# Kernel tuning notes

Measured on AMD Instinct MI355X. Metric: run time of the kernel, lower is better.

The kernel has to match this reference:

```python
import jax, jax.numpy as jnp
import numpy as np

N_NODES = 100000
N_EDGES = 1600000
INPUT_DIM = 128
HIDDEN = 128
OUTPUT_DIM = 2
NUM_LAYERS = 2
MAX_RECURSION = 10
TAU_THRESHOLD = 0.005


def setup_inputs() -> dict:
    key = jax.random.key(0)
    ks = jax.random.split(key, 16)
    s = 0.05
    x = jax.random.normal(ks[0], (N_NODES, INPUT_DIM), dtype=jnp.float32)
    edge_index = jax.random.randint(ks[1], (2, N_EDGES), 0, N_NODES, dtype=jnp.int64)
    W_in = jax.random.normal(ks[2], (HIDDEN, INPUT_DIM), dtype=jnp.float32) * s
    b_in = jax.random.normal(ks[3], (HIDDEN,), dtype=jnp.float32) * s
    Wd = jax.random.normal(ks[4], (NUM_LAYERS, HIDDEN, 2 * HIDDEN), dtype=jnp.float32) * s
    bd = jax.random.normal(ks[5], (NUM_LAYERS, HIDDEN), dtype=jnp.float32) * s
    Wt = jax.random.normal(ks[6], (1, HIDDEN), dtype=jnp.float32) * s
    bt = jax.random.normal(ks[7], (1,), dtype=jnp.float32) * s
    W_ih = jax.random.normal(ks[8], (3 * HIDDEN, HIDDEN), dtype=jnp.float32) * s
    W_hh = jax.random.normal(ks[9], (3 * HIDDEN, HIDDEN), dtype=jnp.float32) * s
    b_ih = jax.random.normal(ks[10], (3 * HIDDEN,), dtype=jnp.float32) * s
    b_hh = jax.random.normal(ks[11], (3 * HIDDEN,), dtype=jnp.float32) * s
    Wo = jax.random.normal(ks[12], (OUTPUT_DIM, HIDDEN), dtype=jnp.float32) * s
    bo = jax.random.normal(ks[13], (OUTPUT_DIM,), dtype=jnp.float32) * s
    return dict(x=x, edge_index=edge_index, W_in=W_in, b_in=b_in, Wd=Wd, bd=bd,
                Wt=Wt, bt=bt, W_ih=W_ih, W_hh=W_hh, b_ih=b_ih, b_hh=b_hh, Wo=Wo, bo=bo)


def _gru_cell(x, h, W_ih, W_hh, b_ih, b_hh):
    # torch.nn.GRUCell math
    gi = x @ W_ih.T + b_ih  # [N, 3H]
    gh = h @ W_hh.T + b_hh
    i_r, i_z, i_n = jnp.split(gi, 3, axis=-1)
    h_r, h_z, h_n = jnp.split(gh, 3, axis=-1)
    r = jax.nn.sigmoid(i_r + h_r)
    z = jax.nn.sigmoid(i_z + h_z)
    n = jnp.tanh(i_n + r * h_n)
    return (1.0 - z) * n + z * h


def reference(x, edge_index, W_in, b_in, Wd, bd, Wt, bt, W_ih, W_hh, b_ih, b_hh, Wo, bo):
    N = x.shape[0]
    row, col = edge_index[0], edge_index[1]
    h = jax.nn.relu(x @ W_in.T + b_in)  # [N, H]
    tau = None
    for l in range(NUM_LAYERS):
        diff = jnp.abs(h[row] - h[col])  # [E, H]
        diff_agg = jax.ops.segment_sum(diff, row, num_segments=N)  # [N, H]
        h = jax.nn.relu(jnp.concatenate([h, diff_agg], axis=-1) @ Wd[l].T + bd[l])
        tau = jax.nn.softplus(h @ Wt.T + bt).squeeze(-1)  # [N]
        # n_updates = clamp(floor(1/tau), max=MAX_RECURSION); node updated iff
        # n_updates > 0 and tau < TAU_THRESHOLD. The original inner loop applies
        # gru(diff_agg[i], h[i]) with the ORIGINAL h[i] each iteration, so repeated
        # application is idempotent -> single masked GRU step is exact same math.
        n_updates = jnp.minimum(jnp.floor(1.0 / tau).astype(jnp.int32), MAX_RECURSION)
        mask = (n_updates > 0) & (tau < TAU_THRESHOLD)
        h_gru = _gru_cell(diff_agg, h, W_ih, W_hh, b_ih, b_hh)
        h = jnp.where(mask[:, None], h_gru, h)
    out = h @ Wo.T + bo  # [N, OUTPUT_DIM]
    return out, tau
```

## Files before the change

kernel.cpp:

```cpp
#include <hip/hip_runtime.h>
#include <cstdint>
#include <cstddef>

#define HID 128
#define BSHIFT 7
#define NSB 256
#define MAXB 4096


__global__ __launch_bounds__(256)
void ecount_kernel(const int* __restrict__ row, int* __restrict__ countsT,
                   int E, int nbuck,
                   const float* __restrict__ W_in, const float* __restrict__ Wd,
                   const float* __restrict__ W_ih, const float* __restrict__ W_hh,
                   float* __restrict__ WinT, float* __restrict__ WdT0,
                   float* __restrict__ WdT1, float* __restrict__ WihT,
                   float* __restrict__ WhhT) {
  for (int i = blockIdx.x * 256 + threadIdx.x; i < 180224; i += NSB * 256) {
    int j = i;
    if (j < 16384) { int r = j >> 7, c = j & 127; WinT[c * 128 + r] = W_in[j]; continue; }
    j -= 16384;
    if (j < 32768) { int r = j >> 8, c = j & 255; WdT0[c * 128 + r] = Wd[j]; continue; }
    j -= 32768;
    if (j < 32768) { int r = j >> 8, c = j & 255; WdT1[c * 128 + r] = Wd[32768 + j]; continue; }
    j -= 32768;
    if (j < 49152) { int r = j >> 7, c = j & 127; WihT[c * 384 + r] = W_ih[j]; continue; }
    j -= 49152;
    { int r = j >> 7, c = j & 127; WhhT[c * 384 + r] = W_hh[j]; }
  }
  __shared__ int lh[1024];
  int b = blockIdx.x;
  for (int i = threadIdx.x; i < nbuck; i += 256) lh[i] = 0;
  __syncthreads();
  int per = (E + NSB - 1) / NSB;
  int s = b * per, e = min(s + per, E);
  for (int i = s + (int)threadIdx.x; i < e; i += 256)
    atomicAdd(&lh[row[i] >> BSHIFT], 1);
  __syncthreads();
  for (int i = threadIdx.x; i < nbuck; i += 256) countsT[i * NSB + b] = lh[i];
}

__global__ __launch_bounds__(NSB)
void bprefix_kernel(int* __restrict__ countsT, int* __restrict__ btotal, int nbuck) {
  __shared__ int sd[NSB];
  int bk = blockIdx.x;
  int t = threadIdx.x;
  int v = countsT[bk * NSB + t];
  sd[t] = v;
  __syncthreads();
  for (int off = 1; off < NSB; off <<= 1) {
    int u = (t >= off) ? sd[t - off] : 0;
    __syncthreads();
    sd[t] += u;
    __syncthreads();
  }
  countsT[bk * NSB + t] = sd[t] - v;
  if (t == NSB - 1) btotal[bk] = sd[t];
}

__global__ __launch_bounds__(1024)
void bstart_kernel(const int* __restrict__ btotal, int* __restrict__ bstart,
                   int* __restrict__ offsets, int N, int nbuck) {
  __shared__ int sd[1024];
  int t = threadIdx.x;
  int v = (t < nbuck) ? btotal[t] : 0;
  sd[t] = v;
  __syncthreads();
  for (int off = 1; off < 1024; off <<= 1) {
    int u = (t >= off) ? sd[t - off] : 0;
    __syncthreads();
    sd[t] += u;
    __syncthreads();
  }
  if (t < nbuck) bstart[t] = sd[t] - v;
  if (t == nbuck - 1) { bstart[nbuck] = sd[t]; offsets[N] = sd[t]; }
}

__global__ __launch_bounds__(256)
void escatter_kernel(const int* __restrict__ row, const int* __restrict__ col,
                     const int* __restrict__ countsT, const int* __restrict__ bstart,
                     int2* __restrict__ ebuf, int E, int nbuck) {
  __shared__ int lcur[1024];
  int b = blockIdx.x;
  for (int i = threadIdx.x; i < nbuck; i += 256)
    lcur[i] = bstart[i] + countsT[i * NSB + b];
  __syncthreads();
  int per = (E + NSB - 1) / NSB;
  int s = b * per, e = min(s + per, E);
  for (int i = s + (int)threadIdx.x; i < e; i += 256) {
    int r = row[i], c = col[i];
    int pos = atomicAdd(&lcur[r >> BSHIFT], 1);
    ebuf[pos] = make_int2(r, c);
  }
}

__global__ __launch_bounds__(256)
void bsort_gin_kernel(const int2* __restrict__ ebuf, const int* __restrict__ bstart,
                      int* __restrict__ offsets, int* __restrict__ csr_col,
                      int N, int nbuck,
                      const float* __restrict__ A, const float* __restrict__ BT,
                      const float* __restrict__ bias, float* __restrict__ C, int G) {
  __shared__ union {
    struct { int cnt[128]; int off[128]; int cur[128]; int lcol[MAXB]; } s;
    struct { float As[32][68]; float Bs[32][128]; } g;
  } sm;
  int bid = blockIdx.x;
  int tid = threadIdx.x;
  if (bid < nbuck) {
    int bk = bid;
    int s = bstart[bk], e = bstart[bk + 1];
    int m = e - s;
    if (tid < 128) sm.s.cnt[tid] = 0;
    __syncthreads();
    for (int i = s + tid; i < e; i += 256)
      atomicAdd(&sm.s.cnt[ebuf[i].x & 127], 1);
    __syncthreads();
    if (tid < 128) sm.s.off[tid] = sm.s.cnt[tid];
    __syncthreads();
    for (int d = 1; d < 128; d <<= 1) {
      int v = 0;
      if (tid < 128 && tid >= d) v = sm.s.off[tid - d];
      __syncthreads();
      if (tid < 128) sm.s.off[tid] += v;
      __syncthreads();
    }
    if (tid < 128) {
      sm.s.cur[tid] = sm.s.off[tid] - sm.s.cnt[tid];
      int node = (bk << BSHIFT) + tid;
      if (node < N) offsets[node] = s + sm.s.off[tid] - sm.s.cnt[tid];
    }
    __syncthreads();
    if (m <= MAXB) {
      for (int i = s + tid; i < e; i += 256) {
        int2 rc = ebuf[i];
        int pos = atomicAdd(&sm.s.cur[rc.x & 127], 1);
        sm.s.lcol[pos] = rc.y;
      }
      __syncthreads();
      if (tid < 128) {
        int b0 = sm.s.off[tid] - sm.s.cnt[tid], b1 = sm.s.off[tid];
        for (int i = b0 + 1; i < b1; ++i) {
          int key = sm.s.lcol[i];
          int j = i - 1;
          while (j >= b0 && sm.s.lcol[j] > key) { sm.s.lcol[j + 1] = sm.s.lcol[j]; --j; }
          sm.s.lcol[j + 1] = key;
        }
      }
      __syncthreads();
      for (int i = tid; i < m; i += 256) csr_col[s + i] = sm.s.lcol[i];
    } else {
      for (int i = s + tid; i < e; i += 256) {
        int2 rc = ebuf[i];
        int pos = atomicAdd(&sm.s.cur[rc.x & 127], 1);
        csr_col[s + pos] = rc.y;
      }
    }
    return;
  }
  int tile = bid - nbuck;
  if (tile >= G) return;
  int tx = tid & 31;
  int ty = tid >> 5;
  int i0 = tile * 64;
  int M = N;
  float acc[8][4] = {};
  for (int kc = 0; kc < 4; ++kc) {
    int ksrc = kc * 32;
    #pragma unroll
    for (int q = 0; q < 2; ++q) {
      int f = q * 256 + tid;
      int i = f >> 3;
      int kq = (f & 7) << 2;
      int ig = i0 + i; if (ig >= M) ig = M - 1;
      float4 v = *(const float4*)(A + (size_t)ig * HID + ksrc + kq);
      sm.g.As[kq + 0][i] = v.x; sm.g.As[kq + 1][i] = v.y;
      sm.g.As[kq + 2][i] = v.z; sm.g.As[kq + 3][i] = v.w;
    }
    #pragma unroll
    for (int q = 0; q < 4; ++q) {
      int f = q * 256 + tid;
      int k = f >> 5; int c4 = (f & 31) << 2;
      *(float4*)&sm.g.Bs[k][c4] = *(const float4*)(BT + (size_t)(ksrc + k) * HID + c4);
    }
    __syncthreads();
    #pragma unroll
    for (int k = 0; k < 32; ++k) {
      float a[8];
      const float4* ap = (const float4*)&sm.g.As[k][ty * 8];
      float4 a0 = ap[0], a1 = ap[1];
      a[0]=a0.x; a[1]=a0.y; a[2]=a0.z; a[3]=a0.w;
      a[4]=a1.x; a[5]=a1.y; a[6]=a1.z; a[7]=a1.w;
      float4 b4 = *(const float4*)&sm.g.Bs[k][tx * 4];
      #pragma unroll
      for (int r = 0; r < 8; ++r) {
        acc[r][0] = fmaf(a[r], b4.x, acc[r][0]);
        acc[r][1] = fmaf(a[r], b4.y, acc[r][1]);
        acc[r][2] = fmaf(a[r], b4.z, acc[r][2]);
        acc[r][3] = fmaf(a[r], b4.w, acc[r][3]);
      }
    }
    __syncthreads();
  }
  float4 bias4 = *(const float4*)(bias + tx * 4);
  #pragma unroll
  for (int r = 0; r < 8; ++r) {
    int row = i0 + ty * 8 + r;
    if (row >= M) continue;
    float4 v4 = make_float4(fmaxf(acc[r][0] + bias4.x, 0.f),
                            fmaxf(acc[r][1] + bias4.y, 0.f),
                            fmaxf(acc[r][2] + bias4.z, 0.f),
                            fmaxf(acc[r][3] + bias4.w, 0.f));
    *(float4*)(C + (size_t)row * HID + tx * 4) = v4;
  }
}

__device__ __forceinline__ void agg_one_node(const float* __restrict__ h,
                                             const int* __restrict__ offsets,
                                             const int* __restrict__ csr_col,
                                             float* __restrict__ diff, int node) {
  int lane = threadIdx.x & 63;
  int start = offsets[node], end = offsets[node + 1];
  int deg = end - start;
  const float2* hrow = (const float2*)(h + (size_t)node * HID);
  float2 hv = hrow[lane];
  float a0 = 0.f, a1 = 0.f;

  int batch = min(deg, 64);
  int myc = (lane < batch) ? csr_col[start + lane] : 0;
  int j = 0;
  for (; j + 16 <= batch; j += 16) {
    const float2* p0 = (const float2*)(h + (size_t)__shfl(myc, j + 0) * HID);
    const float2* p1 = (const float2*)(h + (size_t)__shfl(myc, j + 1) * HID);
    const float2* p2 = (const float2*)(h + (size_t)__shfl(myc, j + 2) * HID);
    const float2* p3 = (const float2*)(h + (size_t)__shfl(myc, j + 3) * HID);
    const float2* p4 = (const float2*)(h + (size_t)__shfl(myc, j + 4) * HID);
    const float2* p5 = (const float2*)(h + (size_t)__shfl(myc, j + 5) * HID);
    const float2* p6 = (const float2*)(h + (size_t)__shfl(myc, j + 6) * HID);
    const float2* p7 = (const float2*)(h + (size_t)__shfl(myc, j + 7) * HID);
    const float2* q0 = (const float2*)(h + (size_t)__shfl(myc, j + 8) * HID);
    const float2* q1 = (const float2*)(h + (size_t)__shfl(myc, j + 9) * HID);
    const float2* q2 = (const float2*)(h + (size_t)__shfl(myc, j + 10) * HID);
    const float2* q3 = (const float2*)(h + (size_t)__shfl(myc, j + 11) * HID);
    const float2* q4 = (const float2*)(h + (size_t)__shfl(myc, j + 12) * HID);
    const float2* q5 = (const float2*)(h + (size_t)__shfl(myc, j + 13) * HID);
    const float2* q6 = (const float2*)(h + (size_t)__shfl(myc, j + 14) * HID);
    const float2* q7 = (const float2*)(h + (size_t)__shfl(myc, j + 15) * HID);
    float2 x0 = p0[lane], x1 = p1[lane], x2 = p2[lane], x3 = p3[lane];
    float2 x4 = p4[lane], x5 = p5[lane], x6 = p6[lane], x7 = p7[lane];
    float2 y0 = q0[lane], y1 = q1[lane], y2 = q2[lane], y3 = q3[lane];
    float2 y4 = q4[lane], y5 = q5[lane], y6 = q6[lane], y7 = q7[lane];
    a0 += fabsf(hv.x - x0.x) + fabsf(hv.x - x1.x) + fabsf(hv.x - x2.x) + fabsf(hv.x - x3.x)
        + fabsf(hv.x - x4.x) + fabsf(hv.x - x5.x) + fabsf(hv.x - x6.x) + fabsf(hv.x - x7.x);
    a1 += fabsf(hv.y - x0.y) + fabsf(hv.y - x1.y) + fabsf(hv.y - x2.y) + fabsf(hv.y - x3.y)
        + fabsf(hv.y - x4.y) + fabsf(hv.y - x5.y) + fabsf(hv.y - x6.y) + fabsf(hv.y - x7.y);
    a0 += fabsf(hv.x - y0.x) + fabsf(hv.x - y1.x) + fabsf(hv.x - y2.x) + fabsf(hv.x - y3.x)
        + fabsf(hv.x - y4.x) + fabsf(hv.x - y5.x) + fabsf(hv.x - y6.x) + fabsf(hv.x - y7.x);
    a1 += fabsf(hv.y - y0.y) + fabsf(hv.y - y1.y) + fabsf(hv.y - y2.y) + fabsf(hv.y - y3.y)
        + fabsf(hv.y - y4.y) + fabsf(hv.y - y5.y) + fabsf(hv.y - y6.y) + fabsf(hv.y - y7.y);
  }
  for (; j + 8 <= batch; j += 8) {
    const float2* p0 = (const float2*)(h + (size_t)__shfl(myc, j + 0) * HID);
    const float2* p1 = (const float2*)(h + (size_t)__shfl(myc, j + 1) * HID);
    const float2* p2 = (const float2*)(h + (size_t)__shfl(myc, j + 2) * HID);
    const float2* p3 = (const float2*)(h + (size_t)__shfl(myc, j + 3) * HID);
    const float2* p4 = (const float2*)(h + (size_t)__shfl(myc, j + 4) * HID);
    const float2* p5 = (const float2*)(h + (size_t)__shfl(myc, j + 5) * HID);
    const float2* p6 = (const float2*)(h + (size_t)__shfl(myc, j + 6) * HID);
    const float2* p7 = (const float2*)(h + (size_t)__shfl(myc, j + 7) * HID);
    float2 x0 = p0[lane], x1 = p1[lane], x2 = p2[lane], x3 = p3[lane];
    float2 x4 = p4[lane], x5 = p5[lane], x6 = p6[lane], x7 = p7[lane];
    a0 += fabsf(hv.x - x0.x) + fabsf(hv.x - x1.x) + fabsf(hv.x - x2.x) + fabsf(hv.x - x3.x)
        + fabsf(hv.x - x4.x) + fabsf(hv.x - x5.x) + fabsf(hv.x - x6.x) + fabsf(hv.x - x7.x);
    a1 += fabsf(hv.y - x0.y) + fabsf(hv.y - x1.y) + fabsf(hv.y - x2.y) + fabsf(hv.y - x3.y)
        + fabsf(hv.y - x4.y) + fabsf(hv.y - x5.y) + fabsf(hv.y - x6.y) + fabsf(hv.y - x7.y);
  }
  for (; j < batch; ++j) {
    const float2* p = (const float2*)(h + (size_t)__shfl(myc, j) * HID);
    float2 x = p[lane];
    a0 += fabsf(hv.x - x.x);
    a1 += fabsf(hv.y - x.y);
  }
  for (int e = start + 64; e < end; ++e) {
    const float2* p = (const float2*)(h + (size_t)csr_col[e] * HID);
    float2 x = p[lane];
    a0 += fabsf(hv.x - x.x);
    a1 += fabsf(hv.y - x.y);
  }
  *(float2*)(diff + (size_t)node * HID + 2 * lane) = make_float2(a0, a1);
}

__global__ __launch_bounds__(256, 4)
void fused_ap1_kernel(const float* __restrict__ h, const int* __restrict__ offsets,
                      const int* __restrict__ csr_col, float* __restrict__ diff,
                      const float* __restrict__ BT, float* __restrict__ Cpart,
                      int M, int G) {
  __shared__ float As[32][68];
  __shared__ float Bs[32][128];
  int bid = blockIdx.x;
  int tid = threadIdx.x;
  int q17 = bid / 17, r17 = bid % 17;
  if (r17 == 0 && q17 < G) {
    int tx = tid & 31;
    int ty = tid >> 5;
    int i0 = q17 * 64;
    float acc[8][4] = {};
    for (int kc = 0; kc < 4; ++kc) {
      int ksrc = kc * 32;
      #pragma unroll
      for (int q = 0; q < 2; ++q) {
        int f = q * 256 + tid;
        int i = f >> 3;
        int kq = (f & 7) << 2;
        int ig = i0 + i; if (ig >= M) ig = M - 1;
        float4 v = *(const float4*)(h + (size_t)ig * HID + ksrc + kq);
        As[kq + 0][i] = v.x; As[kq + 1][i] = v.y;
        As[kq + 2][i] = v.z; As[kq + 3][i] = v.w;
      }
      #pragma unroll
      for (int q = 0; q < 4; ++q) {
        int f = q * 256 + tid;
        int k = f >> 5; int c4 = (f & 31) << 2;
        *(float4*)&Bs[k][c4] = *(const float4*)(BT + (size_t)(ksrc + k) * HID + c4);
      }
      __syncthreads();
      #pragma unroll
      for (int k = 0; k < 32; ++k) {
        float a[8];
        const float4* ap = (const float4*)&As[k][ty * 8];
        float4 a0 = ap[0], a1 = ap[1];
        a[0]=a0.x; a[1]=a0.y; a[2]=a0.z; a[3]=a0.w;
        a[4]=a1.x; a[5]=a1.y; a[6]=a1.z; a[7]=a1.w;
        float4 b4 = *(const float4*)&Bs[k][tx * 4];
        #pragma unroll
        for (int r = 0; r < 8; ++r) {
          acc[r][0] = fmaf(a[r], b4.x, acc[r][0]);
          acc[r][1] = fmaf(a[r], b4.y, acc[r][1]);
          acc[r][2] = fmaf(a[r], b4.z, acc[r][2]);
          acc[r][3] = fmaf(a[r], b4.w, acc[r][3]);
        }
      }
      __syncthreads();
    }
    #pragma unroll
    for (int r = 0; r < 8; ++r) {
      int row = i0 + ty * 8 + r;
      if (row < M) {
        *(float4*)(Cpart + (size_t)row * HID + tx * 4) =
            make_float4(acc[r][0], acc[r][1], acc[r][2], acc[r][3]);
      }
    }
  } else {
    int ngemm_before = (bid + 16) / 17; if (ngemm_before > G) ngemm_before = G;
    int aidx = bid - ngemm_before;
    int wave = tid >> 6;
    int node = aidx * 4 + wave;
    if (node >= M) return;
    agg_one_node(h, offsets, csr_col, diff, node);
  }
}

template<bool OUT>
__global__ __launch_bounds__(256)
void gemm_p2_kernel(const float* __restrict__ A2, const float* __restrict__ BT,
                    const float* __restrict__ bias, float* __restrict__ C,
                    int M,
                    const float* __restrict__ Wt, const float* __restrict__ bt,
                    float* __restrict__ tau_out, int* __restrict__ mlist,
                    int* __restrict__ mcount,
                    const float* __restrict__ Wo, const float* __restrict__ bo,
                    float* __restrict__ outp) {
  __shared__ float As[32][68];
  __shared__ float Bs[32][128];
  __shared__ float taured[64];
  int tid = threadIdx.x;
  int tx = tid & 31;
  int ty = tid >> 5;
  int i0 = blockIdx.x * 64;
  float acc[8][4] = {};
  #pragma unroll
  for (int r = 0; r < 8; ++r) {
    int row = i0 + ty * 8 + r;
    if (row < M) {
      float4 v = *(const float4*)(C + (size_t)row * HID + tx * 4);
      acc[r][0] = v.x; acc[r][1] = v.y; acc[r][2] = v.z; acc[r][3] = v.w;
    }
  }
  for (int kc = 4; kc < 8; ++kc) {
    int ksrc = (kc & 3) * 32;
    int kglob = kc * 32;
    #pragma unroll
    for (int q = 0; q < 2; ++q) {
      int f = q * 256 + tid;
      int i = f >> 3;
      int kq = (f & 7) << 2;
      int ig = i0 + i; if (ig >= M) ig = M - 1;
      float4 v = *(const float4*)(A2 + (size_t)ig * HID + ksrc + kq);
      As[kq + 0][i] = v.x; As[kq + 1][i] = v.y;
      As[kq + 2][i] = v.z; As[kq + 3][i] = v.w;
    }
    #pragma unroll
    for (int q = 0; q < 4; ++q) {
      int f = q * 256 + tid;
      int k = f >> 5; int c4 = (f & 31) << 2;
      *(float4*)&Bs[k][c4] = *(const float4*)(BT + (size_t)(kglob + k) * HID + c4);
    }
    __syncthreads();
    #pragma unroll
    for (int k = 0; k < 32; ++k) {
      float a[8];
      const float4* ap = (const float4*)&As[k][ty * 8];
      float4 a0 = ap[0], a1 = ap[1];
      a[0]=a0.x; a[1]=a0.y; a[2]=a0.z; a[3]=a0.w;
      a[4]=a1.x; a[5]=a1.y; a[6]=a1.z; a[7]=a1.w;
      float4 b4 = *(const float4*)&Bs[k][tx * 4];
      #pragma unroll
      for (int r = 0; r < 8; ++r) {
        acc[r][0] = fmaf(a[r], b4.x, acc[r][0]);
        acc[r][1] = fmaf(a[r], b4.y, acc[r][1]);
        acc[r][2] = fmaf(a[r], b4.z, acc[r][2]);
        acc[r][3] = fmaf(a[r], b4.w, acc[r][3]);
      }
    }
    __syncthreads();
  }

  float4 bias4 = *(const float4*)(bias + tx * 4);
  float bias_r[4] = {bias4.x, bias4.y, bias4.z, bias4.w};
  float4 w4 = *(const float4*)(Wt + tx * 4);
  float wt_r[4] = {w4.x, w4.y, w4.z, w4.w};
  float4 wo0 = make_float4(0.f, 0.f, 0.f, 0.f);
  float4 wo1 = make_float4(0.f, 0.f, 0.f, 0.f);
  if constexpr (OUT) {
    wo0 = *(const float4*)(Wo + tx * 4);
    wo1 = *(const float4*)(Wo + 128 + tx * 4);
  }
  #pragma unroll
  for (int r = 0; r < 8; ++r) {
    int row = i0 + ty * 8 + r;
    bool ok = row < M;
    float v0 = fmaxf(acc[r][0] + bias_r[0], 0.f);
    float v1 = fmaxf(acc[r][1] + bias_r[1], 0.f);
    float v2 = fmaxf(acc[r][2] + bias_r[2], 0.f);
    float v3 = fmaxf(acc[r][3] + bias_r[3], 0.f);
    if (ok) {
      float4 v4 = make_float4(v0, v1, v2, v3);
      *(float4*)(C + (size_t)row * HID + tx * 4) = v4;
    }
    if constexpr (OUT) {
      float o0 = v0 * wo0.x + v1 * wo0.y + v2 * wo0.z + v3 * wo0.w;
      float o1 = v0 * wo1.x + v1 * wo1.y + v2 * wo1.z + v3 * wo1.w;
      o0 += __shfl_down(o0, 16, 32); o1 += __shfl_down(o1, 16, 32);
      o0 += __shfl_down(o0, 8, 32);  o1 += __shfl_down(o1, 8, 32);
      o0 += __shfl_down(o0, 4, 32);  o1 += __shfl_down(o1, 4, 32);
      o0 += __shfl_down(o0, 2, 32);  o1 += __shfl_down(o1, 2, 32);
      o0 += __shfl_down(o0, 1, 32);  o1 += __shfl_down(o1, 1, 32);
      if (tx == 0 && ok) {
        outp[(size_t)row * 2 + 0] = o0 + bo[0];
        outp[(size_t)row * 2 + 1] = o1 + bo[1];
      }
    }
    {
      float pf = v0 * wt_r[0];
      pf = fmaf(v1, wt_r[1], pf);
      pf = fmaf(v2, wt_r[2], pf);
      pf = fmaf(v3, wt_r[3], pf);
      pf += __shfl_down(pf, 16, 32);
      pf += __shfl_down(pf, 8, 32);
      pf += __shfl_down(pf, 4, 32);
      pf += __shfl_down(pf, 2, 32);
      pf += __shfl_down(pf, 1, 32);
      if (tx == 0) taured[ty * 8 + r] = pf;
    }
  }
  __syncthreads();
  if (tid < 64) {
    int row = i0 + tid;
    if (row < M) {
      float pre = taured[tid] + bt[0];
      float tau = (pre > 20.f) ? pre : log1pf(expf(pre));
      tau_out[row] = tau;
      if (tau < 0.005f && (1.0f / tau) < 2147483648.0f) {
        int pos = atomicAdd(mcount, 1);
        mlist[pos] = row;
      }
    }
  }
}

template<bool LAST>
__global__ __launch_bounds__(512)
void gru_kernel(const float* __restrict__ diff, float* __restrict__ h,
                const int* __restrict__ list, const int* __restrict__ count,
                const float* __restrict__ WihT, const float* __restrict__ WhhT,
                const float* __restrict__ b_ih, const float* __restrict__ b_hh,
                const float* __restrict__ Wo, const float* __restrict__ bo,
                float* __restrict__ outp) {
  int cnt = *count;
  int base = blockIdx.x * 32;
  if (base >= cnt) return;
  __shared__ float dl[32][HID];
  __shared__ float hl[32][HID];
  __shared__ int ids[32];
  __shared__ float osum[32][2][2];
  int tid = threadIdx.x;
  if (tid < 32) ids[tid] = (base + tid < cnt) ? list[base + tid] : -1;
  __syncthreads();
  #pragma unroll
  for (int q = 0; q < 8; ++q) {
    int f = q * 512 + tid;
    int r = f >> 7, c = f & 127;
    int id = ids[r];
    int src = (id >= 0) ? id : 0;
    dl[r][c] = diff[(size_t)src * HID + c];
    hl[r][c] = h[(size_t)src * HID + c];
  }
  __syncthreads();
  int tx = tid & 127, ty = tid >> 7;
  float air[8] = {}, aiz[8] = {}, ain[8] = {}, ahr[8] = {}, ahz[8] = {}, ahn[8] = {};
  for (int k = 0; k < HID; ++k) {
    float wir = WihT[k * 384 + tx];
    float wiz = WihT[k * 384 + 128 + tx];
    float win = WihT[k * 384 + 256 + tx];
    float whr = WhhT[k * 384 + tx];
    float whz = WhhT[k * 384 + 128 + tx];
    float whn = WhhT[k * 384 + 256 + tx];
    #pragma unroll
    for (int r = 0; r < 8; ++r) {
      float dk = dl[ty * 8 + r][k];
      float hk = hl[ty * 8 + r][k];
      air[r] = fmaf(dk, wir, air[r]);
      aiz[r] = fmaf(dk, wiz, aiz[r]);
      ain[r] = fmaf(dk, win, ain[r]);
      ahr[r] = fmaf(hk, whr, ahr[r]);
      ahz[r] = fmaf(hk, whz, ahz[r]);
      ahn[r] = fmaf(hk, whn, ahn[r]);
    }
  }
  float bir = b_ih[tx], biz = b_ih[128 + tx], bin = b_ih[256 + tx];
  float bhr = b_hh[tx], bhz = b_hh[128 + tx], bhn = b_hh[256 + tx];
  float wol0 = 0.f, wol1 = 0.f;
  if constexpr (LAST) { wol0 = Wo[tx]; wol1 = Wo[128 + tx]; }
  #pragma unroll
  for (int r = 0; r < 8; ++r) {
    int id = ids[ty * 8 + r];
    float rg = 1.f / (1.f + expf(-((air[r] + bir) + (ahr[r] + bhr))));
    float z  = 1.f / (1.f + expf(-((aiz[r] + biz) + (ahz[r] + bhz))));
    float n  = tanhf((ain[r] + bin) + rg * (ahn[r] + bhn));
    float hv = hl[ty * 8 + r][tx];
    float hnew = (1.f - z) * n + z * hv;
    if (id >= 0) h[(size_t)id * HID + tx] = hnew;
    if constexpr (LAST) {
      float p0 = hnew * wol0;
      float p1 = hnew * wol1;
      p0 += __shfl_down(p0, 32, 64); p1 += __shfl_down(p1, 32, 64);
      p0 += __shfl_down(p0, 16, 64); p1 += __shfl_down(p1, 16, 64);
      p0 += __shfl_down(p0, 8, 64);  p1 += __shfl_down(p1, 8, 64);
      p0 += __shfl_down(p0, 4, 64);  p1 += __shfl_down(p1, 4, 64);
      p0 += __shfl_down(p0, 2, 64);  p1 += __shfl_down(p1, 2, 64);
      p0 += __shfl_down(p0, 1, 64);  p1 += __shfl_down(p1, 1, 64);
      if ((tx & 63) == 0) {
        osum[ty * 8 + r][tx >> 6][0] = p0;
        osum[ty * 8 + r][tx >> 6][1] = p1;
      }
    }
  }
  if constexpr (LAST) {
    __syncthreads();
    if (tid < 32) {
      int id = ids[tid];
      if (id >= 0) {
        outp[(size_t)id * 2 + 0] = osum[tid][0][0] + osum[tid][1][0] + bo[0];
        outp[(size_t)id * 2 + 1] = osum[tid][0][1] + osum[tid][1][1] + bo[1];
      }
    }
  }
}

extern "C" void kernel_launch(void* const* d_in, const int* in_sizes, int n_in,
                              void* d_out, int out_size, void* d_ws, size_t ws_size,
                              hipStream_t stream) {
  const float* x    = (const float*)d_in[0];
  const int*   ei   = (const int*)d_in[1];
  const float* W_in = (const float*)d_in[2];
  const float* b_in = (const float*)d_in[3];
  const float* Wd   = (const float*)d_in[4];
  const float* bd   = (const float*)d_in[5];
  const float* Wt   = (const float*)d_in[6];
  const float* bt   = (const float*)d_in[7];
  const float* W_ih = (const float*)d_in[8];
  const float* W_hh = (const float*)d_in[9];
  const float* b_ih = (const float*)d_in[10];
  const float* b_hh = (const float*)d_in[11];
  const float* Wo   = (const float*)d_in[12];
  const float* bo   = (const float*)d_in[13];

  const int N = in_sizes[0] / HID;
  const int E = in_sizes[1] / 2;
  const int* rowp = ei;
  const int* colp = ei + E;
  const int nbuck = (N + (1 << BSHIFT) - 1) >> BSHIFT;

  char* p = (char*)d_ws;
  auto alloc = [&](size_t bytes) { void* r = (void*)p; p += (bytes + 255) & ~(size_t)255; return r; };
  float* hA     = (float*)alloc((size_t)N * HID * 4);
  float* hB     = (float*)alloc((size_t)N * HID * 4);
  float* diff   = (float*)alloc((size_t)N * HID * 4);
  float* WinT   = (float*)alloc(128 * 128 * 4);
  float* WdT0   = (float*)alloc(256 * 128 * 4);
  float* WdT1   = (float*)alloc(256 * 128 * 4);
  float* WihT   = (float*)alloc(128 * 384 * 4);
  float* WhhT   = (float*)alloc(128 * 384 * 4);
  float* tau0   = (float*)alloc((size_t)N * 4);
  int*   list   = (int*)alloc((size_t)N * 4);
  int*   count  = (int*)alloc(256);
  int*   countsT= (int*)alloc((size_t)1024 * NSB * 4);
  int*   btotal = (int*)alloc(1024 * 4);
  int*   bstart = (int*)alloc(1028 * 4);
  int*   offs   = (int*)alloc(((size_t)N + 1) * 4);
  int*   csrcol = (int*)alloc((size_t)E * 4);
  int2*  ebuf   = (int2*)alloc((size_t)E * 8);

  float* out_ptr = (float*)d_out;
  float* tau_out = (float*)d_out + (size_t)N * 2;

  hipMemsetAsync(count, 0, 8, stream);

  ecount_kernel<<<NSB, 256, 0, stream>>>(rowp, countsT, E, nbuck,
                                         W_in, Wd, W_ih, W_hh,
                                         WinT, WdT0, WdT1, WihT, WhhT);
  bprefix_kernel<<<nbuck, NSB, 0, stream>>>(countsT, btotal, nbuck);
  bstart_kernel<<<1, 1024, 0, stream>>>(btotal, bstart, offs, N, nbuck);
  escatter_kernel<<<NSB, 256, 0, stream>>>(rowp, colp, countsT, bstart, ebuf, E, nbuck);

  const int G = (N + 63) / 64;
  const int agg_groups = (N + 3) / 4;
  const int fused_blocks = G + agg_groups;
  const int gru_blocks = (N + 31) / 32;

  bsort_gin_kernel<<<nbuck + G, 256, 0, stream>>>(
      ebuf, bstart, offs, csrcol, N, nbuck, x, WinT, b_in, hA, G);

  fused_ap1_kernel<<<fused_blocks, 256, 0, stream>>>(
      hA, offs, csrcol, diff, WdT0, hB, N, G);
  gemm_p2_kernel<false><<<G, 256, 0, stream>>>(
      diff, WdT0, bd, hB, N, Wt, bt, tau0, list, count,
      nullptr, nullptr, nullptr);
  gru_kernel<false><<<gru_blocks, 512, 0, stream>>>(
      diff, hB, list, count, WihT, WhhT, b_ih, b_hh, nullptr, nullptr, nullptr);

  fused_ap1_kernel<<<fused_blocks, 256, 0, stream>>>(
      hB, offs, csrcol, diff, WdT1, hA, N, G);
  gemm_p2_kernel<true><<<G, 256, 0, stream>>>(
      diff, WdT1, bd + 128, hA, N, Wt, bt, tau_out, list, count + 1,
      Wo, bo, out_ptr);
  gru_kernel<true><<<gru_blocks, 512, 0, stream>>>(
      diff, hA, list, count + 1, WihT, WhhT, b_ih, b_hh, Wo, bo, out_ptr);
}
```

Measured before the change: 726.2 us.

## Fuse masked GRU update into dense GEMM epilogue, drop separate GRU kernels

Removes the global masked-node list, its atomic counter and memset, and the two gru_kernel launches. Each GEMM block now gathers its own masked rows into shared memory and runs the GRU cell for them one row at a time, using 128 threads, right after computing tau. This saves two launches plus a global list round trip, since masked nodes are likely rare. The cost is that a block with masked rows serializes per-row GRU work, reloading the weights each time while half the threads sit idle, which could hurt if many nodes are masked.

```diff
diff --git a/kernel.cpp b/kernel.cpp
--- a/kernel.cpp
+++ b/kernel.cpp
@@ -365,17 +365,24 @@
                     const float* __restrict__ bias, float* __restrict__ C,
                     int M,
                     const float* __restrict__ Wt, const float* __restrict__ bt,
-                    float* __restrict__ tau_out, int* __restrict__ mlist,
-                    int* __restrict__ mcount,
+                    float* __restrict__ tau_out,
+                    const float* __restrict__ WihT, const float* __restrict__ WhhT,
+                    const float* __restrict__ b_ih, const float* __restrict__ b_hh,
                     const float* __restrict__ Wo, const float* __restrict__ bo,
                     float* __restrict__ outp) {
   __shared__ float As[32][68];
   __shared__ float Bs[32][128];
   __shared__ float taured[64];
+  __shared__ float dl_s[HID];
+  __shared__ float hl_s[HID];
+  __shared__ int mrows[64];
+  __shared__ int mcnt_s;
+  __shared__ float osum_s[2][2];
   int tid = threadIdx.x;
   int tx = tid & 31;
   int ty = tid >> 5;
   int i0 = blockIdx.x * 64;
+  if (tid == 0) mcnt_s = 0;
   float acc[8][4] = {};
   #pragma unroll
   for (int r = 0; r < 8; ++r) {
@@ -480,97 +487,68 @@
       float tau = (pre > 20.f) ? pre : log1pf(expf(pre));
       tau_out[row] = tau;
       if (tau < 0.005f && (1.0f / tau) < 2147483648.0f) {
-        int pos = atomicAdd(mcount, 1);
-        mlist[pos] = row;
-      }
-    }
-  }
-}
-
-template<bool LAST>
-__global__ __launch_bounds__(512)
-void gru_kernel(const float* __restrict__ diff, float* __restrict__ h,
-                const int* __restrict__ list, const int* __restrict__ count,
-                const float* __restrict__ WihT, const float* __restrict__ WhhT,
-                const float* __restrict__ b_ih, const float* __restrict__ b_hh,
-                const float* __restrict__ Wo, const float* __restrict__ bo,
-                float* __restrict__ outp) {
-  int cnt = *count;
-  int base = blockIdx.x * 32;
-  if (base >= cnt) return;
-  __shared__ float dl[32][HID];
-  __shared__ float hl[32][HID];
-  __shared__ int ids[32];
-  __shared__ float osum[32][2][2];
-  int tid = threadIdx.x;
-  if (tid < 32) ids[tid] = (base + tid < cnt) ? list[base + tid] : -1;
+        int pos = atomicAdd(&mcnt_s, 1);
+        mrows[pos] = tid;
+      }
+    }
+  }
   __syncthreads();
-  #pragma unroll
-  for (int q = 0; q < 8; ++q) {
-    int f = q * 512 + tid;
-    int r = f >> 7, c = f & 127;
-    int id = ids[r];
-    int src = (id >= 0) ? id : 0;
-    dl[r][c] = diff[(size_t)src * HID + c];
-    hl[r][c] = h[(size_t)src * HID + c];
-  }
-  __syncthreads();
-  int tx = tid & 127, ty = tid >> 7;
-  float air[8] = {}, aiz[8] = {}, ain[8] = {}, ahr[8] = {}, ahz[8] = {}, ahn[8] = {};
-  for (int k = 0; k < HID; ++k) {
-    float wir = WihT[k * 384 + tx];
-    float wiz = WihT[k * 384 + 128 + tx];
-    float win = WihT[k * 384 + 256 + tx];
-    float whr = WhhT[k * 384 + tx];
-    float whz = WhhT[k * 384 + 128 + tx];
-    float whn = WhhT[k * 384 + 256 + tx];
-    #pragma unroll
-    for (int r = 0; r < 8; ++r) {
-      float dk = dl[ty * 8 + r][k];
-      float hk = hl[ty * 8 + r][k];
-      air[r] = fmaf(dk, wir, air[r]);
-      aiz[r] = fmaf(dk, wiz, aiz[r]);
-      ain[r] = fmaf(dk, win, ain[r]);
-      ahr[r] = fmaf(hk, whr, ahr[r]);
-      ahz[r] = fmaf(hk, whz, ahz[r]);
-      ahn[r] = fmaf(hk, whn, ahn[r]);
-    }
-  }
-  float bir = b_ih[tx], biz = b_ih[128 + tx], bin = b_ih[256 + tx];
-  float bhr = b_hh[tx], bhz = b_hh[128 + tx], bhn = b_hh[256 + tx];
-  float wol0 = 0.f, wol1 = 0.f;
-  if constexpr (LAST) { wol0 = Wo[tx]; wol1 = Wo[128 + tx]; }
-  #pragma unroll
-  for (int r = 0; r < 8; ++r) {
-    int id = ids[ty * 8 + r];
-    float rg = 1.f / (1.f + expf(-((air[r] + bir) + (ahr[r] + bhr))));
-    float z  = 1.f / (1.f + expf(-((aiz[r] + biz) + (ahz[r] + bhz))));
-    float n  = tanhf((ain[r] + bin) + rg * (ahn[r] + bhn));
-    float hv = hl[ty * 8 + r][tx];
-    float hnew = (1.f - z) * n + z * hv;
-    if (id >= 0) h[(size_t)id * HID + tx] = hnew;
-    if constexpr (LAST) {
-      float p0 = hnew * wol0;
-      float p1 = hnew * wol1;
-      p0 += __shfl_down(p0, 32, 64); p1 += __shfl_down(p1, 32, 64);
-      p0 += __shfl_down(p0, 16, 64); p1 += __shfl_down(p1, 16, 64);
-      p0 += __shfl_down(p0, 8, 64);  p1 += __shfl_down(p1, 8, 64);
-      p0 += __shfl_down(p0, 4, 64);  p1 += __shfl_down(p1, 4, 64);
-      p0 += __shfl_down(p0, 2, 64);  p1 += __shfl_down(p1, 2, 64);
-      p0 += __shfl_down(p0, 1, 64);  p1 += __shfl_down(p1, 1, 64);
-      if ((tx & 63) == 0) {
-        osum[ty * 8 + r][tx >> 6][0] = p0;
-        osum[ty * 8 + r][tx >> 6][1] = p1;
-      }
-    }
-  }
-  if constexpr (LAST) {
-    __syncthreads();
-    if (tid < 32) {
-      int id = ids[tid];
-      if (id >= 0) {
-        outp[(size_t)id * 2 + 0] = osum[tid][0][0] + osum[tid][1][0] + bo[0];
-        outp[(size_t)id * 2 + 1] = osum[tid][0][1] + osum[tid][1][1] + bo[1];
+  int mc = mcnt_s;
+  for (int mi = 0; mi < mc; ++mi) {
+    int lrow = mrows[mi];
+    int grow = i0 + lrow;
+    if (tid < 128) {
+      dl_s[tid] = A2[(size_t)grow * HID + tid];
+      hl_s[tid] = C[(size_t)grow * HID + tid];
+    }
+    __syncthreads();
+    if (tid < 128) {
+      int txg = tid;
+      float air = 0.f, aiz = 0.f, ain_ = 0.f, ahr = 0.f, ahz = 0.f, ahn = 0.f;
+      for (int k = 0; k < HID; ++k) {
+        float wir = WihT[k * 384 + txg];
+        float wiz = WihT[k * 384 + 128 + txg];
+        float win = WihT[k * 384 + 256 + txg];
+        float whr = WhhT[k * 384 + txg];
+        float whz = WhhT[k * 384 + 128 + txg];
+        float whn = WhhT[k * 384 + 256 + txg];
+        float dk = dl_s[k];
+        float hk = hl_s[k];
+        air = fmaf(dk, wir, air);
+        aiz = fmaf(dk, wiz, aiz);
+        ain_ = fmaf(dk, win, ain_);
+        ahr = fmaf(hk, whr, ahr);
+        ahz = fmaf(hk, whz, ahz);
+        ahn = fmaf(hk, whn, ahn);
+      }
+      float bir = b_ih[txg], biz = b_ih[128 + txg], bin = b_ih[256 + txg];
+      float bhr = b_hh[txg], bhz = b_hh[128 + txg], bhn = b_hh[256 + txg];
+      float rg = 1.f / (1.f + expf(-((air + bir) + (ahr + bhr))));
+      float z  = 1.f / (1.f + expf(-((aiz + biz) + (ahz + bhz))));
+      float n  = tanhf((ain_ + bin) + rg * (ahn + bhn));
+      float hv = hl_s[txg];
+      float hnew = (1.f - z) * n + z * hv;
+      C[(size_t)grow * HID + txg] = hnew;
+      if constexpr (OUT) {
+        float p0 = hnew * Wo[txg];
+        float p1 = hnew * Wo[128 + txg];
+        p0 += __shfl_down(p0, 32, 64); p1 += __shfl_down(p1, 32, 64);
+        p0 += __shfl_down(p0, 16, 64); p1 += __shfl_down(p1, 16, 64);
+        p0 += __shfl_down(p0, 8, 64);  p1 += __shfl_down(p1, 8, 64);
+        p0 += __shfl_down(p0, 4, 64);  p1 += __shfl_down(p1, 4, 64);
+        p0 += __shfl_down(p0, 2, 64);  p1 += __shfl_down(p1, 2, 64);
+        p0 += __shfl_down(p0, 1, 64);  p1 += __shfl_down(p1, 1, 64);
+        if ((txg & 63) == 0) {
+          osum_s[txg >> 6][0] = p0;
+          osum_s[txg >> 6][1] = p1;
+        }
+      }
+    }
+    __syncthreads();
+    if constexpr (OUT) {
+      if (tid == 0) {
+        outp[(size_t)grow * 2 + 0] = osum_s[0][0] + osum_s[1][0] + bo[0];
+        outp[(size_t)grow * 2 + 1] = osum_s[0][1] + osum_s[1][1] + bo[1];
       }
     }
   }
@@ -611,8 +589,6 @@
   float* WihT   = (float*)alloc(128 * 384 * 4);
   float* WhhT   = (float*)alloc(128 * 384 * 4);
   float* tau0   = (float*)alloc((size_t)N * 4);
-  int*   list   = (int*)alloc((size_t)N * 4);
-  int*   count  = (int*)alloc(256);
   int*   countsT= (int*)alloc((size_t)1024 * NSB * 4);
   int*   btotal = (int*)alloc(1024 * 4);
   int*   bstart = (int*)alloc(1028 * 4);
@@ -623,8 +599,6 @@
   float* out_ptr = (float*)d_out;
   float* tau_out = (float*)d_out + (size_t)N * 2;
 
-  hipMemsetAsync(count, 0, 8, stream);
-
   ecount_kernel<<<NSB, 256, 0, stream>>>(rowp, countsT, E, nbuck,
                                          W_in, Wd, W_ih, W_hh,
                                          WinT, WdT0, WdT1, WihT, WhhT);
@@ -635,7 +609,6 @@
   const int G = (N + 63) / 64;
   const int agg_groups = (N + 3) / 4;
   const int fused_blocks = G + agg_groups;
-  const int gru_blocks = (N + 31) / 32;
 
   bsort_gin_kernel<<<nbuck + G, 256, 0, stream>>>(
       ebuf, bstart, offs, csrcol, N, nbuck, x, WinT, b_in, hA, G);
@@ -643,16 +616,12 @@
   fused_ap1_kernel<<<fused_blocks, 256, 0, stream>>>(
       hA, offs, csrcol, diff, WdT0, hB, N, G);
   gemm_p2_kernel<false><<<G, 256, 0, stream>>>(
-      diff, WdT0, bd, hB, N, Wt, bt, tau0, list, count,
-      nullptr, nullptr, nullptr);
-  gru_kernel<false><<<gru_blocks, 512, 0, stream>>>(
-      diff, hB, list, count, WihT, WhhT, b_ih, b_hh, nullptr, nullptr, nullptr);
+      diff, WdT0, bd, hB, N, Wt, bt, tau0,
+      WihT, WhhT, b_ih, b_hh, nullptr, nullptr, nullptr);
 
   fused_ap1_kernel<<<fused_blocks, 256, 0, stream>>>(
       hB, offs, csrcol, diff, WdT1, hA, N, G);
   gemm_p2_kernel<true><<<G, 256, 0, stream>>>(
-      diff, WdT1, bd + 128, hA, N, Wt, bt, tau_out, list, count + 1,
-      Wo, bo, out_ptr);
-  gru_kernel<true><<<gru_blocks, 512, 0, stream>>>(
-      diff, hA, list, count + 1, WihT, WhhT, b_ih, b_hh, Wo, bo, out_ptr);
-}
+      diff, WdT1, bd + 128, hA, N, Wt, bt, tau_out,
+      WihT, WhhT, b_ih, b_hh, Wo, bo, out_ptr);
+}
```

Result: faster. 654.1 us (-9.9%).
